# Optimization experiments

Hardware: AMD Instinct MI355X
Metric: run time of the kernel (lower is better)

## Reference

```python
import jax, jax.numpy as jnp
import numpy as np

ALPHA = 0.3  # LeakyReLU negative slope
NEG_INF = -1e9


def setup_inputs() -> dict:
    key = jax.random.key(0)
    k1, k2, k3, k4 = jax.random.split(key, 4)
    B, N, C_IN, C_OUT, H = 4, 2048, 128, 128, 4
    node_feats = jax.random.normal(k1, (B, N, C_IN), dtype=jnp.float32)
    # xavier_uniform with gain 1.414 for projection weight [c_out, c_in]
    limit_w = 1.414 * np.sqrt(6.0 / (C_IN + C_OUT))
    W = jax.random.uniform(k2, (C_OUT, C_IN), minval=-limit_w, maxval=limit_w, dtype=jnp.float32)
    b = jnp.zeros((C_OUT,), dtype=jnp.float32)
    c_head = C_OUT // H
    limit_a = 1.414 * np.sqrt(6.0 / (H + 2 * c_head))
    a = jax.random.uniform(k3, (H, 2 * c_head), minval=-limit_a, maxval=limit_a, dtype=jnp.float32)
    return {"node_feats": node_feats, "W": W, "b": b, "a": a}


def reference(node_feats, W, b, a):
    B, N, _ = node_feats.shape
    H, two_c = a.shape
    c = two_c // 2
    # dynamic adjacency: cosine similarity, sigmoid > 0.5  <=>  sim > 0
    nf = node_feats / jnp.maximum(jnp.linalg.norm(node_feats, axis=-1, keepdims=True), 1e-12)
    sim = jnp.einsum('bid,bjd->bij', nf, nf)            # [B,N,N]
    mask = sim > 0.0                                     # adjacency (sigmoid(sim) > 0.5)
    # projection -> per-head features [B,N,H,c]
    h = (node_feats @ W.T + b).reshape(B, N, H, c)
    # edge score a . [h_i, h_j] decomposes into left/right parts
    a_l, a_r = a[:, :c], a[:, c:]                        # [H,c] each
    s_l = jnp.einsum('bnhc,hc->bnh', h, a_l)             # [B,N,H]
    s_r = jnp.einsum('bnhc,hc->bnh', h, a_r)             # [B,N,H]
    logits = jax.nn.leaky_relu(s_l[:, :, None, :] + s_r[:, None, :, :], ALPHA)  # [B,N,N,H]
    attn = jnp.where(mask[..., None], logits, NEG_INF)
    probs = jax.nn.softmax(attn, axis=2)                 # softmax over source nodes j
    # dropout is identity in eval mode
    out = jnp.einsum('bijh,bjhc->bihc', probs, h)
    return out.reshape(B, N, -1)                         # concat heads
```

## Files before the change

### kernel.cpp

```cpp
#include <hip/hip_runtime.h>
#include <cstdint>
#include <cstddef>

typedef float v16f __attribute__((ext_vector_type(16)));
typedef short v8s  __attribute__((ext_vector_type(8)));

#define MFMA32(A,B,C) __builtin_amdgcn_mfma_f32_32x32x16_bf16((A),(B),(C),0,0,0)
#define THRU 1e-3f
#define SEG 16

__device__ __forceinline__ unsigned f2bf(float f) {
  unsigned u = __builtin_bit_cast(unsigned, f);
  u += 0x7FFFu + ((u >> 16) & 1u);
  return u >> 16;
}
__device__ __forceinline__ float bf2f(unsigned us) {
  return __builtin_bit_cast(float, us << 16);
}
__device__ __forceinline__ void gload16(const void* g, void* l) {
  __builtin_amdgcn_global_load_lds(
      (const __attribute__((address_space(1))) void*)g,
      (__attribute__((address_space(3))) void*)l, 16, 0, 0);
}

__global__ __launch_bounds__(256) void gat_prep(
    const float* __restrict__ nf, const float* __restrict__ Wm,
    const float* __restrict__ bias, const float* __restrict__ aw,
    unsigned short* __restrict__ nfh, unsigned short* __restrict__ nfm,
    unsigned short* __restrict__ ht,
    float* __restrict__ EFl, float* __restrict__ EFrp)
{
  __shared__ float xl[32][132];
  const int tid = threadIdx.x;
  const int row = tid & 31, g = tid >> 5;
  const int r0 = blockIdx.x * 32;
  const int b = r0 >> 11, n0 = r0 & 2047;
  const int d0 = g * 16;

  float x[16];
  {
    const float* xp = nf + (size_t)(r0 + row) * 128 + d0;
#pragma unroll
    for (int q = 0; q < 4; ++q) {
      float4 v = *(const float4*)(xp + 4 * q);
      x[4*q+0] = v.x; x[4*q+1] = v.y; x[4*q+2] = v.z; x[4*q+3] = v.w;
    }
  }
  {
    unsigned hu[16], mu[16];
#pragma unroll
    for (int q = 0; q < 16; ++q) {
      xl[row][d0 + q] = x[q];
      unsigned hb = f2bf(x[q]); float hf = bf2f(hb);
      unsigned mb = f2bf(x[q] - hf);
      hu[q] = hb; mu[q] = mb;
    }
    const size_t to = ((size_t)(b * 64 + (n0 >> 5)) * 8 + g) * 512 + row * 8;
    uint4 p0, p1;
    p0.x = hu[0] | (hu[1] << 16);  p0.y = hu[2] | (hu[3] << 16);
    p0.z = hu[4] | (hu[5] << 16);  p0.w = hu[6] | (hu[7] << 16);
    p1.x = hu[8] | (hu[9] << 16);  p1.y = hu[10] | (hu[11] << 16);
    p1.z = hu[12] | (hu[13] << 16); p1.w = hu[14] | (hu[15] << 16);
    *(uint4*)(nfh + to) = p0; *(uint4*)(nfh + to + 256) = p1;
    p0.x = mu[0] | (mu[1] << 16);  p0.y = mu[2] | (mu[3] << 16);
    p0.z = mu[4] | (mu[5] << 16);  p0.w = mu[6] | (mu[7] << 16);
    p1.x = mu[8] | (mu[9] << 16);  p1.y = mu[10] | (mu[11] << 16);
    p1.z = mu[12] | (mu[13] << 16); p1.w = mu[14] | (mu[15] << 16);
    *(uint4*)(nfm + to) = p0; *(uint4*)(nfm + to + 256) = p1;
  }
  __syncthreads();

  float acc[16];
  const int ob = g * 16;
#pragma unroll
  for (int o = 0; o < 16; ++o) acc[o] = bias[ob + o];
  for (int dd = 0; dd < 128; dd += 4) {
    float4 xq = *(const float4*)&xl[row][dd];
#pragma unroll
    for (int o = 0; o < 16; ++o) {
      float4 wq = *(const float4*)(Wm + (size_t)(ob + o) * 128 + dd);
      acc[o] = fmaf(xq.x, wq.x, acc[o]);
      acc[o] = fmaf(xq.y, wq.y, acc[o]);
      acc[o] = fmaf(xq.z, wq.z, acc[o]);
      acc[o] = fmaf(xq.w, wq.w, acc[o]);
    }
  }
#pragma unroll
  for (int o = 0; o < 16; ++o)
    ht[((size_t)b * 128 + ob + o) * 2048 + n0 + row] = (unsigned short)f2bf(acc[o]);

  const int hh = g >> 1, cb = (g & 1) * 16;
  float sl = 0.f, sr = 0.f;
#pragma unroll
  for (int o = 0; o < 16; ++o) {
    sl = fmaf(acc[o], aw[hh * 64 + cb + o], sl);
    sr = fmaf(acc[o], aw[hh * 64 + 32 + cb + o], sr);
  }
  sl += __shfl_xor(sl, 32, 64);
  sr += __shfl_xor(sr, 32, 64);
  if (!(g & 1)) {
    const float L2E = 1.4426950408889634f;
    float El = exp2f(sl * L2E), Fl = exp2f(sl * (0.3f * L2E));
    float Er = exp2f(sr * L2E), Fr = exp2f(sr * (0.3f * L2E));
    size_t nn = (size_t)(r0 + row);
    EFl[nn * 8 + hh]     = El;
    EFl[nn * 8 + 4 + hh] = Fl;
    EFrp[nn * 8 + (hh >> 1) * 4 + (hh & 1) * 2]     = Er;
    EFrp[nn * 8 + (hh >> 1) * 4 + (hh & 1) * 2 + 1] = Fr;
  }
}

__global__ __launch_bounds__(256) void gat_mask(
    const unsigned short* __restrict__ nfh, const unsigned short* __restrict__ nfm,
    unsigned* __restrict__ mask, unsigned* __restrict__ list,
    unsigned* __restrict__ lcnt)
{
  const int tid = threadIdx.x, lane = tid & 63, wv = tid >> 6;
  const int li = lane & 31, hi = lane >> 5;
  const int blk = blockIdx.x;
  const int jb = blk & 31, t = blk >> 5;
  const int ib = t & 15, b = t >> 4;
  const int i0 = ib * 128 + wv * 32;
  const int j0 = jb * 64;
  const int wid = blk * 4 + wv;

  const size_t lbyte = (size_t)lane * 8;
  const size_t tiB  = ((size_t)(b * 64 + (i0 >> 5)) * 8) * 512 + lbyte;
  const size_t tjA0 = ((size_t)(b * 64 + (j0 >> 5)) * 8) * 512 + lbyte;
  const size_t tjA1 = tjA0 + 4096;

  v8s BH[8], BM[8];
#pragma unroll
  for (int kc = 0; kc < 8; ++kc) {
    BH[kc] = *(const v8s*)(nfh + tiB + kc * 512);
    BM[kc] = *(const v8s*)(nfm + tiB + kc * 512);
  }

  v16f S0, S1;
#pragma unroll
  for (int r = 0; r < 16; ++r) { S0[r] = 0.f; S1[r] = 0.f; }
#pragma unroll
  for (int kc = 0; kc < 8; ++kc) {
    v8s A0h = *(const v8s*)(nfh + tjA0 + kc * 512);
    v8s A1h = *(const v8s*)(nfh + tjA1 + kc * 512);
    v8s A0m = *(const v8s*)(nfm + tjA0 + kc * 512);
    v8s A1m = *(const v8s*)(nfm + tjA1 + kc * 512);
    S0 = MFMA32(A0h, BH[kc], S0);
    S1 = MFMA32(A1h, BH[kc], S1);
    S0 = MFMA32(A0h, BM[kc], S0);
    S1 = MFMA32(A1h, BM[kc], S1);
    S0 = MFMA32(A0m, BH[kc], S0);
    S1 = MFMA32(A1m, BH[kc], S1);
  }

  unsigned u0 = 0, u1 = 0;
  float mn = 1e30f;
  const int sh = hi * 4;
#pragma unroll
  for (int r = 0; r < 16; ++r) {
    const int jlc = (r & 3) + 8 * (r >> 2);
    const unsigned bit = (1u << jlc) << sh;
    if (S0[r] > 0.f) u0 |= bit;
    if (S1[r] > 0.f) u1 |= bit;
    mn = fminf(mn, fabsf(S0[r]));
    mn = fminf(mn, fabsf(S1[r]));
  }
  {
    unsigned f0 = u0 | (unsigned)__shfl_xor((int)u0, 32, 64);
    unsigned f1 = u1 | (unsigned)__shfl_xor((int)u1, 32, 64);
    if (hi == 0) {
      mask[(size_t)(b * 64 + jb * 2)     * 2048 + i0 + li] = f0;
      mask[(size_t)(b * 64 + jb * 2 + 1) * 2048 + i0 + li] = f1;
    }
  }

  int wcount = 0;
  if (__ballot(mn < THRU)) {
#pragma unroll
    for (int sub = 0; sub < 2; ++sub) {
#pragma unroll
      for (int r = 0; r < 16; ++r) {
        const int jl = (r & 3) + 8 * (r >> 2) + 4 * hi;
        const float s = sub ? S1[r] : S0[r];
        const bool f = fabsf(s) < THRU;
        unsigned long long bal = __ballot(f);
        if (bal) {
          if (f) {
            int pos = wcount + (int)__popcll(bal & ((1ull << lane) - 1ull));
            if (pos < SEG)
              list[wid * SEG + pos] =
                  (unsigned)((b << 22) | ((i0 + li) << 11) | (j0 + sub * 32 + jl));
          }
          wcount += (int)__popcll(bal);
        }
      }
    }
    if (wcount > SEG) wcount = SEG;
  }
  if (lane == 0) lcnt[wid] = (unsigned)wcount;
}

__global__ __launch_bounds__(256) void gat_fix(
    const float* __restrict__ nf, const unsigned* __restrict__ list,
    const unsigned* __restrict__ lcnt, unsigned* __restrict__ mask)
{
  const unsigned t = blockIdx.x * 256 + threadIdx.x;
  const unsigned seg = t >> 4, slot = t & (SEG - 1);
  if (slot >= lcnt[seg]) return;
  const unsigned e = list[t];
  const int b = e >> 22, i = (e >> 11) & 2047, j = e & 2047;
  const float* xi = nf + ((size_t)b * 2048 + i) * 128;
  const float* xj = nf + ((size_t)b * 2048 + j) * 128;
  double acc = 0.0;
#pragma unroll 8
  for (int k = 0; k < 128; k += 4) {
    float4 a = *(const float4*)(xi + k);
    float4 c = *(const float4*)(xj + k);
    acc = fma((double)a.x, (double)c.x, acc);
    acc = fma((double)a.y, (double)c.y, acc);
    acc = fma((double)a.z, (double)c.z, acc);
    acc = fma((double)a.w, (double)c.w, acc);
  }
  unsigned* w = &mask[(size_t)(b * 64 + (j >> 5)) * 2048 + i];
  const unsigned bit = 1u << (j & 31);
  if (acc > 0.0) atomicOr(w, bit); else atomicAnd(w, ~bit);
}

#define PVBLK(pw, h, smv)                                                      \
  {                                                                            \
    auto q0 = __builtin_amdgcn_permlane32_swap((int)pw[0], (int)pw[2], false, false); \
    auto q1 = __builtin_amdgcn_permlane32_swap((int)pw[1], (int)pw[3], false, false); \
    auto q2 = __builtin_amdgcn_permlane32_swap((int)pw[4], (int)pw[6], false, false); \
    auto q3 = __builtin_amdgcn_permlane32_swap((int)pw[5], (int)pw[7], false, false); \
    uint4 c0, c1;                                                              \
    c0.x = (unsigned)q0[0]; c0.y = (unsigned)q1[0];                            \
    c0.z = (unsigned)q0[1]; c0.w = (unsigned)q1[1];                            \
    c1.x = (unsigned)q2[0]; c1.y = (unsigned)q3[0];                            \
    c1.z = (unsigned)q2[1]; c1.w = (unsigned)q3[1];                            \
    v8s P0 = __builtin_bit_cast(v8s, c0);                                      \
    v8s P1 = __builtin_bit_cast(v8s, c1);                                      \
    const int cc = (h) * 32 + li;                                              \
    const char* vr = (smv) + cc * 256;                                         \
    const int cx = cc & 15;                                                    \
    v8s V0 = *(const v8s*)(vr + ((((it2 << 2) + hi) ^ cx) << 4));              \
    v8s V1 = *(const v8s*)(vr + ((((it2 << 2) + 2 + hi) ^ cx) << 4));          \
    acc[h] = MFMA32(P0, V0, acc[h]);                                           \
    acc[h] = MFMA32(P1, V1, acc[h]);                                           \
  }

template<int CH>
__global__ __launch_bounds__(256, 2) void gat_attn(
    const unsigned short* __restrict__ ht, const float* __restrict__ EFl,
    const float* __restrict__ EFrp, const unsigned* __restrict__ mask,
    float* __restrict__ nump, float* __restrict__ denp)
{
  constexpr int JPC = 2048 / CH;
  constexpr int H = JPC >> 7;
  constexpr int MW = JPC >> 5;
  __shared__ __align__(16) char sm[2][18432];

  const int tid = threadIdx.x, lane = tid & 63, wv = tid >> 6;
  const int li = lane & 31, hi = lane >> 5;

  const int blk = blockIdx.x;
  const int x = blk & 7, y = blk >> 3;
  const int ig = y & 15;
  const int combo = x * CH + (y >> 4);
  const int hp2 = combo & 1;
  const int r2 = combo >> 1;
  const int ch = r2 % CH, b = r2 / CH;

  const size_t nb = (size_t)b * 2048;
  const int i0 = ig * 128 + wv * 32;
  const int j0 = ch * JPC;

  float EL[2], FL[2];
  {
    const float* p = EFl + (nb + i0 + li) * 8 + 2 * hp2;
    float2 e = *(const float2*)p;
    float2 f = *(const float2*)(p + 4);
    EL[0] = e.x; EL[1] = e.y; FL[0] = f.x; FL[1] = f.y;
  }

  unsigned mw[MW];
#pragma unroll
  for (int q = 0; q < MW; ++q)
    mw[q] = mask[(size_t)(b * 64 + (j0 >> 5) + q) * 2048 + i0 + li] >> (hi * 4);

  v16f acc[2];
#pragma unroll
  for (int h = 0; h < 2; ++h)
#pragma unroll
    for (int r = 0; r < 16; ++r) acc[h][r] = 0.f;
  float den[2] = {0.f, 0.f};

  auto STAGE = [&](int h0, int p) {
    const int jbase = j0 + (h0 << 7);
    const size_t cbase = (size_t)b * 128 + (hp2 << 6);
#pragma unroll
    for (int s = 0; s < 4; ++s) {
      const int L = s * 4096 + tid * 16;
      const int c = L >> 8, gs = (L >> 4) & 15;
      const int g = gs ^ (c & 15);
      gload16((const char*)ht + (((cbase + c) * 2048 + jbase) << 1) + (g << 4),
              sm[p] + L);
    }
    if (tid < 128)
      gload16((const char*)EFrp + (size_t)(nb + jbase + tid) * 32 + (hp2 << 4),
              sm[p] + 16384 + tid * 16);
  };

  STAGE(0, 0);
  __syncthreads();

#pragma unroll
  for (int h0 = 0; h0 < H; ++h0) {
    const int p = h0 & 1;
    if (h0) __syncthreads();
    if (h0 + 1 < H) STAGE(h0 + 1, p ^ 1);

#pragma unroll
    for (int it2 = 0; it2 < 4; ++it2) {
      const char* Eb = sm[p] + 16384 + (it2 << 9);
      const unsigned mh = mw[(h0 << 2) + it2];
      unsigned pA[8], pB[8];
#pragma unroll
      for (int rp = 0; rp < 8; ++rp) {
        const int r0 = 2 * rp;
        const int jl0c = (r0 & 3) + 8 * (r0 >> 2);
        const int nA = (jl0c + 4 * hi) * 16;
        float4 e0 = *(const float4*)(Eb + nA);
        float4 e1 = *(const float4*)(Eb + nA + 16);
        const bool m0 = (mh >> jl0c) & 1;
        const bool m1 = (mh >> (jl0c + 1)) & 1;
        float wA0 = fmaxf(e0.x * EL[0], e0.y * FL[0]); wA0 = m0 ? wA0 : 0.f;
        float wB0 = fmaxf(e0.z * EL[1], e0.w * FL[1]); wB0 = m0 ? wB0 : 0.f;
        float wA1 = fmaxf(e1.x * EL[0], e1.y * FL[0]); wA1 = m1 ? wA1 : 0.f;
        float wB1 = fmaxf(e1.z * EL[1], e1.w * FL[1]); wB1 = m1 ? wB1 : 0.f;
        den[0] += wA0 + wA1;
        den[1] += wB0 + wB1;
        asm("v_cvt_pk_bf16_f32 %0, %1, %2" : "=v"(pA[rp]) : "v"(wA0), "v"(wA1));
        asm("v_cvt_pk_bf16_f32 %0, %1, %2" : "=v"(pB[rp]) : "v"(wB0), "v"(wB1));
      }
      PVBLK(pA, 0, sm[p])
      PVBLK(pB, 1, sm[p])
    }
  }

#pragma unroll
  for (int h = 0; h < 2; ++h) den[h] += __shfl_xor(den[h], 32, 64);

  const size_t obase = ((size_t)b * CH + ch) * 2048 + i0;
#pragma unroll
  for (int h = 0; h < 2; ++h) {
#pragma unroll
    for (int r = 0; r < 16; ++r) {
      const int il = (r & 3) + 8 * (r >> 2) + 4 * hi;
      nump[(obase + il) * 128 + (hp2 * 2 + h) * 32 + li] = acc[h][r];
    }
  }
  if (lane < 32) {
    float2 dv; dv.x = den[0]; dv.y = den[1];
    *(float2*)(denp + (obase + li) * 4 + 2 * hp2) = dv;
  }
}

__global__ __launch_bounds__(256) void gat_reduce(
    const float* __restrict__ nump, const float* __restrict__ denp,
    float* __restrict__ out, const int CH)
{
  const int idx = blockIdx.x * 256 + threadIdx.x;
  const int b = idx >> 18;
  const int rem = idx & 262143;
  const int n = rem >> 7;
  const int col = rem & 127;
  const int h = col >> 5;
  float s = 0.f, d = 0.f;
  for (int ch = 0; ch < CH; ++ch) {
    s += nump[(((size_t)b * CH + ch) * 2048 + n) * 128 + col];
    d += denp[(((size_t)b * CH + ch) * 2048 + n) * 4 + h];
  }
  out[idx] = s / d;
}

extern "C" void kernel_launch(void* const* d_in, const int* in_sizes, int n_in,
                              void* d_out, int out_size, void* d_ws, size_t ws_size,
                              hipStream_t stream) {
  const float* nf   = (const float*)d_in[0];
  const float* Wm   = (const float*)d_in[1];
  const float* bias = (const float*)d_in[2];
  const float* aw   = (const float*)d_in[3];
  float* out = (float*)d_out;
  char* ws = (char*)d_ws;

  unsigned short* nfh  = (unsigned short*)(ws);
  unsigned short* nfm  = (unsigned short*)(ws + 2097152);
  unsigned short* ht   = (unsigned short*)(ws + 4194304);
  float*    EFl  = (float*)(ws + 6291456);
  float*    EFrp = (float*)(ws + 6553600);
  unsigned* mask = (unsigned*)(ws + 6815744);
  unsigned* list = (unsigned*)(ws + 8912896);
  unsigned* lcnt = (unsigned*)(ws + 9437184);
  const size_t o_den = 9469952;

  int CH = 8;
  if (ws_size < o_den + 8ull * 4325376ull) CH = 4;

  float* denp = (float*)(ws + o_den);
  float* nump = (float*)(ws + o_den + (size_t)CH * 131072);

  gat_prep<<<256, 256, 0, stream>>>(nf, Wm, bias, aw, nfh, nfm, ht, EFl, EFrp);
  gat_mask<<<2048, 256, 0, stream>>>(nfh, nfm, mask, list, lcnt);
  gat_fix<<<512, 256, 0, stream>>>(nf, list, lcnt, mask);
  if (CH == 8)
    gat_attn<8><<<1024, 256, 0, stream>>>(ht, EFl, EFrp, mask, nump, denp);
  else
    gat_attn<4><<<512, 256, 0, stream>>>(ht, EFl, EFrp, mask, nump, denp);
  gat_reduce<<<4096, 256, 0, stream>>>(nump, denp, out, CH);
}
```

Baseline: 74.88 us.

## Fuse mask fixup into mask kernel and reduce j-splits inside attention block

The borderline-sign fixup (fp64 dot products for near-zero similarities) moves inline into the mask kernel, which drops the list/count buffers and the separate fix launch. The attention kernel is restructured so each block handles one batch-head pair over 32 rows. Its four waves each take a quarter of the source nodes with per-wave double-buffered async loads synchronised by waitcnt instead of block barriers, then reduce partials through LDS and write normalized output directly. This removes the partial-sum workspace traffic and the reduce kernel, at the cost of divergent fp64 loops in the mask kernel and an LDS reduction at the end of attention.

```diff
diff --git a/kernel.cpp b/kernel.cpp
--- a/kernel.cpp
+++ b/kernel.cpp
@@ -7,7 +7,6 @@
 
 #define MFMA32(A,B,C) __builtin_amdgcn_mfma_f32_32x32x16_bf16((A),(B),(C),0,0,0)
 #define THRU 1e-3f
-#define SEG 16
 
 __device__ __forceinline__ unsigned f2bf(float f) {
   unsigned u = __builtin_bit_cast(unsigned, f);
@@ -28,7 +27,7 @@
     const float* __restrict__ bias, const float* __restrict__ aw,
     unsigned short* __restrict__ nfh, unsigned short* __restrict__ nfm,
     unsigned short* __restrict__ ht,
-    float* __restrict__ EFl, float* __restrict__ EFrp)
+    float* __restrict__ EFl, float* __restrict__ EFh)
 {
   __shared__ float xl[32][132];
   const int tid = threadIdx.x;
@@ -105,24 +104,23 @@
     size_t nn = (size_t)(r0 + row);
     EFl[nn * 8 + hh]     = El;
     EFl[nn * 8 + 4 + hh] = Fl;
-    EFrp[nn * 8 + (hh >> 1) * 4 + (hh & 1) * 2]     = Er;
-    EFrp[nn * 8 + (hh >> 1) * 4 + (hh & 1) * 2 + 1] = Fr;
+    const size_t eo = ((size_t)(b * 4 + hh) * 2048 + (n0 + row)) * 2;
+    EFh[eo]     = Er;
+    EFh[eo + 1] = Fr;
   }
 }
 
 __global__ __launch_bounds__(256) void gat_mask(
     const unsigned short* __restrict__ nfh, const unsigned short* __restrict__ nfm,
-    unsigned* __restrict__ mask, unsigned* __restrict__ list,
-    unsigned* __restrict__ lcnt)
+    const float* __restrict__ nf, unsigned* __restrict__ mask)
 {
-  const int tid = threadIdx.x, lane = tid & 63, wv = tid >> 6;
+  const int tid = threadIdx.x, lane = tid & 63;
   const int li = lane & 31, hi = lane >> 5;
   const int blk = blockIdx.x;
   const int jb = blk & 31, t = blk >> 5;
   const int ib = t & 15, b = t >> 4;
-  const int i0 = ib * 128 + wv * 32;
+  const int i0 = ib * 128 + (tid >> 6) * 32;
   const int j0 = jb * 64;
-  const int wid = blk * 4 + wv;
 
   const size_t lbyte = (size_t)lane * 8;
   const size_t tiB  = ((size_t)(b * 64 + (i0 >> 5)) * 8) * 512 + lbyte;
@@ -165,222 +163,170 @@
     mn = fminf(mn, fabsf(S0[r]));
     mn = fminf(mn, fabsf(S1[r]));
   }
-  {
-    unsigned f0 = u0 | (unsigned)__shfl_xor((int)u0, 32, 64);
-    unsigned f1 = u1 | (unsigned)__shfl_xor((int)u1, 32, 64);
-    if (hi == 0) {
-      mask[(size_t)(b * 64 + jb * 2)     * 2048 + i0 + li] = f0;
-      mask[(size_t)(b * 64 + jb * 2 + 1) * 2048 + i0 + li] = f1;
-    }
-  }
-
-  int wcount = 0;
-  if (__ballot(mn < THRU)) {
+
+  if (mn < THRU) {
+    const float* xi = nf + ((size_t)b * 2048 + i0 + li) * 128;
 #pragma unroll
     for (int sub = 0; sub < 2; ++sub) {
 #pragma unroll
       for (int r = 0; r < 16; ++r) {
-        const int jl = (r & 3) + 8 * (r >> 2) + 4 * hi;
         const float s = sub ? S1[r] : S0[r];
-        const bool f = fabsf(s) < THRU;
-        unsigned long long bal = __ballot(f);
-        if (bal) {
-          if (f) {
-            int pos = wcount + (int)__popcll(bal & ((1ull << lane) - 1ull));
-            if (pos < SEG)
-              list[wid * SEG + pos] =
-                  (unsigned)((b << 22) | ((i0 + li) << 11) | (j0 + sub * 32 + jl));
+        if (fabsf(s) < THRU) {
+          const int jlc = (r & 3) + 8 * (r >> 2);
+          const int j = j0 + sub * 32 + jlc + 4 * hi;
+          const float* xj = nf + ((size_t)b * 2048 + j) * 128;
+          double a = 0.0;
+          for (int k = 0; k < 128; k += 2) {
+            a = fma((double)xi[k],     (double)xj[k],     a);
+            a = fma((double)xi[k + 1], (double)xj[k + 1], a);
           }
-          wcount += (int)__popcll(bal);
+          const unsigned bit = (1u << jlc) << sh;
+          if (sub == 0) u0 = (a > 0.0) ? (u0 | bit) : (u0 & ~bit);
+          else          u1 = (a > 0.0) ? (u1 | bit) : (u1 & ~bit);
         }
       }
     }
-    if (wcount > SEG) wcount = SEG;
-  }
-  if (lane == 0) lcnt[wid] = (unsigned)wcount;
-}
-
-__global__ __launch_bounds__(256) void gat_fix(
-    const float* __restrict__ nf, const unsigned* __restrict__ list,
-    const unsigned* __restrict__ lcnt, unsigned* __restrict__ mask)
-{
-  const unsigned t = blockIdx.x * 256 + threadIdx.x;
-  const unsigned seg = t >> 4, slot = t & (SEG - 1);
-  if (slot >= lcnt[seg]) return;
-  const unsigned e = list[t];
-  const int b = e >> 22, i = (e >> 11) & 2047, j = e & 2047;
-  const float* xi = nf + ((size_t)b * 2048 + i) * 128;
-  const float* xj = nf + ((size_t)b * 2048 + j) * 128;
-  double acc = 0.0;
-#pragma unroll 8
-  for (int k = 0; k < 128; k += 4) {
-    float4 a = *(const float4*)(xi + k);
-    float4 c = *(const float4*)(xj + k);
-    acc = fma((double)a.x, (double)c.x, acc);
-    acc = fma((double)a.y, (double)c.y, acc);
-    acc = fma((double)a.z, (double)c.z, acc);
-    acc = fma((double)a.w, (double)c.w, acc);
-  }
-  unsigned* w = &mask[(size_t)(b * 64 + (j >> 5)) * 2048 + i];
-  const unsigned bit = 1u << (j & 31);
-  if (acc > 0.0) atomicOr(w, bit); else atomicAnd(w, ~bit);
-}
-
-#define PVBLK(pw, h, smv)                                                      \
-  {                                                                            \
-    auto q0 = __builtin_amdgcn_permlane32_swap((int)pw[0], (int)pw[2], false, false); \
-    auto q1 = __builtin_amdgcn_permlane32_swap((int)pw[1], (int)pw[3], false, false); \
-    auto q2 = __builtin_amdgcn_permlane32_swap((int)pw[4], (int)pw[6], false, false); \
-    auto q3 = __builtin_amdgcn_permlane32_swap((int)pw[5], (int)pw[7], false, false); \
-    uint4 c0, c1;                                                              \
-    c0.x = (unsigned)q0[0]; c0.y = (unsigned)q1[0];                            \
-    c0.z = (unsigned)q0[1]; c0.w = (unsigned)q1[1];                            \
-    c1.x = (unsigned)q2[0]; c1.y = (unsigned)q3[0];                            \
-    c1.z = (unsigned)q2[1]; c1.w = (unsigned)q3[1];                            \
-    v8s P0 = __builtin_bit_cast(v8s, c0);                                      \
-    v8s P1 = __builtin_bit_cast(v8s, c1);                                      \
-    const int cc = (h) * 32 + li;                                              \
-    const char* vr = (smv) + cc * 256;                                         \
-    const int cx = cc & 15;                                                    \
-    v8s V0 = *(const v8s*)(vr + ((((it2 << 2) + hi) ^ cx) << 4));              \
-    v8s V1 = *(const v8s*)(vr + ((((it2 << 2) + 2 + hi) ^ cx) << 4));          \
-    acc[h] = MFMA32(P0, V0, acc[h]);                                           \
-    acc[h] = MFMA32(P1, V1, acc[h]);                                           \
-  }
-
-template<int CH>
+  }
+
+  unsigned f0 = u0 | (unsigned)__shfl_xor((int)u0, 32, 64);
+  unsigned f1 = u1 | (unsigned)__shfl_xor((int)u1, 32, 64);
+  if (hi == 0) {
+    mask[(size_t)(b * 64 + jb * 2)     * 2048 + i0 + li] = f0;
+    mask[(size_t)(b * 64 + jb * 2 + 1) * 2048 + i0 + li] = f1;
+  }
+}
+
 __global__ __launch_bounds__(256, 2) void gat_attn(
     const unsigned short* __restrict__ ht, const float* __restrict__ EFl,
-    const float* __restrict__ EFrp, const unsigned* __restrict__ mask,
-    float* __restrict__ nump, float* __restrict__ denp)
+    const float* __restrict__ EFh, const unsigned* __restrict__ mask,
+    float* __restrict__ out)
 {
-  constexpr int JPC = 2048 / CH;
-  constexpr int H = JPC >> 7;
-  constexpr int MW = JPC >> 5;
-  __shared__ __align__(16) char sm[2][18432];
-
+  __shared__ __align__(16) char sm[36864];
   const int tid = threadIdx.x, lane = tid & 63, wv = tid >> 6;
   const int li = lane & 31, hi = lane >> 5;
 
   const int blk = blockIdx.x;
-  const int x = blk & 7, y = blk >> 3;
-  const int ig = y & 15;
-  const int combo = x * CH + (y >> 4);
-  const int hp2 = combo & 1;
-  const int r2 = combo >> 1;
-  const int ch = r2 % CH, b = r2 / CH;
+  const int ig = (blk >> 3) & 63;
+  const int combo = (blk & 7) * 2 + (blk >> 9);
+  const int b = combo >> 2, h = combo & 3;
 
   const size_t nb = (size_t)b * 2048;
-  const int i0 = ig * 128 + wv * 32;
-  const int j0 = ch * JPC;
-
-  float EL[2], FL[2];
-  {
-    const float* p = EFl + (nb + i0 + li) * 8 + 2 * hp2;
-    float2 e = *(const float2*)p;
-    float2 f = *(const float2*)(p + 4);
-    EL[0] = e.x; EL[1] = e.y; FL[0] = f.x; FL[1] = f.y;
-  }
-
-  unsigned mw[MW];
-#pragma unroll
-  for (int q = 0; q < MW; ++q)
-    mw[q] = mask[(size_t)(b * 64 + (j0 >> 5) + q) * 2048 + i0 + li] >> (hi * 4);
-
-  v16f acc[2];
-#pragma unroll
-  for (int h = 0; h < 2; ++h)
-#pragma unroll
-    for (int r = 0; r < 16; ++r) acc[h][r] = 0.f;
-  float den[2] = {0.f, 0.f};
-
+  const int i0 = ig * 32;
+  const int j0w = wv * 512;
+  char* mybase = sm + wv * 9216;
+
+  const float EL = EFl[(nb + i0 + li) * 8 + h];
+  const float FL = EFl[(nb + i0 + li) * 8 + 4 + h];
+
+  unsigned mw[16];
+#pragma unroll
+  for (int q = 0; q < 16; ++q)
+    mw[q] = mask[(size_t)(b * 64 + wv * 16 + q) * 2048 + i0 + li] >> (hi * 4);
+
+  asm volatile("s_waitcnt vmcnt(0)" ::: "memory");
+  __builtin_amdgcn_sched_barrier(0);
+
+  const int vrow = lane >> 3, vgs = lane & 7;
   auto STAGE = [&](int h0, int p) {
-    const int jbase = j0 + (h0 << 7);
-    const size_t cbase = (size_t)b * 128 + (hp2 << 6);
-#pragma unroll
-    for (int s = 0; s < 4; ++s) {
-      const int L = s * 4096 + tid * 16;
-      const int c = L >> 8, gs = (L >> 4) & 15;
-      const int g = gs ^ (c & 15);
-      gload16((const char*)ht + (((cbase + c) * 2048 + jbase) << 1) + (g << 4),
-              sm[p] + L);
-    }
-    if (tid < 128)
-      gload16((const char*)EFrp + (size_t)(nb + jbase + tid) * 32 + (hp2 << 4),
-              sm[p] + 16384 + tid * 16);
+    const int jbase = j0w + (h0 << 6);
+    const size_t srow = (size_t)(b * 128 + h * 32) * 2048 + jbase;
+#pragma unroll
+    for (int q = 0; q < 4; ++q) {
+      const int row = q * 8 + vrow;
+      gload16((const char*)(ht + srow + (size_t)row * 2048 + ((vgs ^ (row & 7)) << 3)),
+              mybase + p * 4608 + q * 1024);
+    }
+    if (lane < 32)
+      gload16((const char*)EFh + ((size_t)(b * 4 + h) * 2048 + jbase) * 8 + lane * 16,
+              mybase + p * 4608 + 4096);
   };
 
   STAGE(0, 0);
-  __syncthreads();
-
-#pragma unroll
-  for (int h0 = 0; h0 < H; ++h0) {
+
+  v16f acc;
+#pragma unroll
+  for (int r = 0; r < 16; ++r) acc[r] = 0.f;
+  float den = 0.f;
+
+#pragma unroll
+  for (int h0 = 0; h0 < 8; ++h0) {
     const int p = h0 & 1;
-    if (h0) __syncthreads();
-    if (h0 + 1 < H) STAGE(h0 + 1, p ^ 1);
-
-#pragma unroll
-    for (int it2 = 0; it2 < 4; ++it2) {
-      const char* Eb = sm[p] + 16384 + (it2 << 9);
-      const unsigned mh = mw[(h0 << 2) + it2];
-      unsigned pA[8], pB[8];
+    if (h0 < 7) {
+      STAGE(h0 + 1, p ^ 1);
+      asm volatile("s_waitcnt vmcnt(5)" ::: "memory");
+    } else {
+      asm volatile("s_waitcnt vmcnt(0)" ::: "memory");
+    }
+    __builtin_amdgcn_sched_barrier(0);
+
+    const char* base = mybase + p * 4608;
+#pragma unroll
+    for (int it2 = 0; it2 < 2; ++it2) {
+      const unsigned mh = mw[h0 * 2 + it2];
+      const char* Eb = base + 4096 + (it2 << 8);
+      unsigned pw[8];
 #pragma unroll
       for (int rp = 0; rp < 8; ++rp) {
         const int r0 = 2 * rp;
         const int jl0c = (r0 & 3) + 8 * (r0 >> 2);
-        const int nA = (jl0c + 4 * hi) * 16;
-        float4 e0 = *(const float4*)(Eb + nA);
-        float4 e1 = *(const float4*)(Eb + nA + 16);
+        const int off = (jl0c + 4 * hi) * 8;
+        float2 e0 = *(const float2*)(Eb + off);
+        float2 e1 = *(const float2*)(Eb + off + 8);
         const bool m0 = (mh >> jl0c) & 1;
         const bool m1 = (mh >> (jl0c + 1)) & 1;
-        float wA0 = fmaxf(e0.x * EL[0], e0.y * FL[0]); wA0 = m0 ? wA0 : 0.f;
-        float wB0 = fmaxf(e0.z * EL[1], e0.w * FL[1]); wB0 = m0 ? wB0 : 0.f;
-        float wA1 = fmaxf(e1.x * EL[0], e1.y * FL[0]); wA1 = m1 ? wA1 : 0.f;
-        float wB1 = fmaxf(e1.z * EL[1], e1.w * FL[1]); wB1 = m1 ? wB1 : 0.f;
-        den[0] += wA0 + wA1;
-        den[1] += wB0 + wB1;
-        asm("v_cvt_pk_bf16_f32 %0, %1, %2" : "=v"(pA[rp]) : "v"(wA0), "v"(wA1));
-        asm("v_cvt_pk_bf16_f32 %0, %1, %2" : "=v"(pB[rp]) : "v"(wB0), "v"(wB1));
+        float w0 = fmaxf(e0.x * EL, e0.y * FL); w0 = m0 ? w0 : 0.f;
+        float w1 = fmaxf(e1.x * EL, e1.y * FL); w1 = m1 ? w1 : 0.f;
+        den += w0 + w1;
+        asm("v_cvt_pk_bf16_f32 %0, %1, %2" : "=v"(pw[rp]) : "v"(w0), "v"(w1));
       }
-      PVBLK(pA, 0, sm[p])
-      PVBLK(pB, 1, sm[p])
-    }
-  }
-
-#pragma unroll
-  for (int h = 0; h < 2; ++h) den[h] += __shfl_xor(den[h], 32, 64);
-
-  const size_t obase = ((size_t)b * CH + ch) * 2048 + i0;
-#pragma unroll
-  for (int h = 0; h < 2; ++h) {
+      auto q0 = __builtin_amdgcn_permlane32_swap((int)pw[0], (int)pw[2], false, false);
+      auto q1 = __builtin_amdgcn_permlane32_swap((int)pw[1], (int)pw[3], false, false);
+      auto q2 = __builtin_amdgcn_permlane32_swap((int)pw[4], (int)pw[6], false, false);
+      auto q3 = __builtin_amdgcn_permlane32_swap((int)pw[5], (int)pw[7], false, false);
+      uint4 c0, c1;
+      c0.x = (unsigned)q0[0]; c0.y = (unsigned)q1[0];
+      c0.z = (unsigned)q0[1]; c0.w = (unsigned)q1[1];
+      c1.x = (unsigned)q2[0]; c1.y = (unsigned)q3[0];
+      c1.z = (unsigned)q2[1]; c1.w = (unsigned)q3[1];
+      v8s P0 = __builtin_bit_cast(v8s, c0);
+      v8s P1 = __builtin_bit_cast(v8s, c1);
+      const char* vr = base + li * 128;
+      const int cx = li & 7;
+      v8s V0 = *(const v8s*)(vr + ((((it2 << 2) + hi) ^ cx) << 4));
+      v8s V1 = *(const v8s*)(vr + ((((it2 << 2) + 2 + hi) ^ cx) << 4));
+      acc = MFMA32(P0, V0, acc);
+      acc = MFMA32(P1, V1, acc);
+    }
+  }
+
+  __syncthreads();
+  if (wv) {
+    float* dst = (float*)sm + (size_t)(wv - 1) * 1088 + lane * 17;
+#pragma unroll
+    for (int r = 0; r < 16; ++r) dst[r] = acc[r];
+    dst[16] = den;
+  }
+  __syncthreads();
+  if (wv == 0) {
+#pragma unroll
+    for (int w = 0; w < 3; ++w) {
+      const float* src = (const float*)sm + (size_t)w * 1088 + lane * 17;
+#pragma unroll
+      for (int r = 0; r < 16; ++r) acc[r] += src[r];
+      den += src[16];
+    }
+    den += __shfl_xor(den, 32, 64);
+    float* dl = (float*)sm + 3 * 1088;
+    if (lane < 32) dl[li] = den;
+    asm volatile("s_waitcnt lgkmcnt(0)" ::: "memory");
+    __builtin_amdgcn_sched_barrier(0);
+    const size_t ob = (nb + i0) * 128 + h * 32 + li;
 #pragma unroll
     for (int r = 0; r < 16; ++r) {
       const int il = (r & 3) + 8 * (r >> 2) + 4 * hi;
-      nump[(obase + il) * 128 + (hp2 * 2 + h) * 32 + li] = acc[h][r];
-    }
-  }
-  if (lane < 32) {
-    float2 dv; dv.x = den[0]; dv.y = den[1];
-    *(float2*)(denp + (obase + li) * 4 + 2 * hp2) = dv;
-  }
-}
-
-__global__ __launch_bounds__(256) void gat_reduce(
-    const float* __restrict__ nump, const float* __restrict__ denp,
-    float* __restrict__ out, const int CH)
-{
-  const int idx = blockIdx.x * 256 + threadIdx.x;
-  const int b = idx >> 18;
-  const int rem = idx & 262143;
-  const int n = rem >> 7;
-  const int col = rem & 127;
-  const int h = col >> 5;
-  float s = 0.f, d = 0.f;
-  for (int ch = 0; ch < CH; ++ch) {
-    s += nump[(((size_t)b * CH + ch) * 2048 + n) * 128 + col];
-    d += denp[(((size_t)b * CH + ch) * 2048 + n) * 4 + h];
-  }
-  out[idx] = s / d;
+      out[ob + (size_t)il * 128] = acc[r] / dl[il];
+    }
+  }
 }
 
 extern "C" void kernel_launch(void* const* d_in, const int* in_sizes, int n_in,
@@ -393,28 +339,14 @@
   float* out = (float*)d_out;
   char* ws = (char*)d_ws;
 
-  unsigned short* nfh  = (unsigned short*)(ws);
-  unsigned short* nfm  = (unsigned short*)(ws + 2097152);
-  unsigned short* ht   = (unsigned short*)(ws + 4194304);
+  unsigned short* nfh = (unsigned short*)(ws);
+  unsigned short* nfm = (unsigned short*)(ws + 2097152);
+  unsigned short* ht  = (unsigned short*)(ws + 4194304);
   float*    EFl  = (float*)(ws + 6291456);
-  float*    EFrp = (float*)(ws + 6553600);
+  float*    EFh  = (float*)(ws + 6553600);
   unsigned* mask = (unsigned*)(ws + 6815744);
-  unsigned* list = (unsigned*)(ws + 8912896);
-  unsigned* lcnt = (unsigned*)(ws + 9437184);
-  const size_t o_den = 9469952;
-
-  int CH = 8;
-  if (ws_size < o_den + 8ull * 4325376ull) CH = 4;
-
-  float* denp = (float*)(ws + o_den);
-  float* nump = (float*)(ws + o_den + (size_t)CH * 131072);
-
-  gat_prep<<<256, 256, 0, stream>>>(nf, Wm, bias, aw, nfh, nfm, ht, EFl, EFrp);
-  gat_mask<<<2048, 256, 0, stream>>>(nfh, nfm, mask, list, lcnt);
-  gat_fix<<<512, 256, 0, stream>>>(nf, list, lcnt, mask);
-  if (CH == 8)
-    gat_attn<8><<<1024, 256, 0, stream>>>(ht, EFl, EFrp, mask, nump, denp);
-  else
-    gat_attn<4><<<512, 256, 0, stream>>>(ht, EFl, EFrp, mask, nump, denp);
-  gat_reduce<<<4096, 256, 0, stream>>>(nump, denp, out, CH);
-}
+
+  gat_prep<<<256, 256, 0, stream>>>(nf, Wm, bias, aw, nfh, nfm, ht, EFl, EFh);
+  gat_mask<<<2048, 256, 0, stream>>>(nfh, nfm, nf, mask);
+  gat_attn<<<1024, 256, 0, stream>>>(ht, EFl, EFh, mask, out);
+}
```

Result: slower. 82.10 us (+9.6%).

## Fuse near-zero similarity fixup into mask kernel and vectorize reduce

Applied to the files above, without the earlier changes.

Drops the separate list/fixup kernel. The mask kernel now recomputes ambiguous near-zero similarity entries in place, in double precision, before writing the mask bits. This removes one launch, the list/count buffers and the atomics. The trade-off is divergent per-lane scalar double loops inside the MFMA kernel, with no cap on how many entries get fixed. The reduce kernel is also switched to float4 loads and stores, with a quarter of the threads.

```diff
diff --git a/kernel.cpp b/kernel.cpp
--- a/kernel.cpp
+++ b/kernel.cpp
@@ -7,7 +7,6 @@
 
 #define MFMA32(A,B,C) __builtin_amdgcn_mfma_f32_32x32x16_bf16((A),(B),(C),0,0,0)
 #define THRU 1e-3f
-#define SEG 16
 
 __device__ __forceinline__ unsigned f2bf(float f) {
   unsigned u = __builtin_bit_cast(unsigned, f);
@@ -112,17 +111,15 @@
 
 __global__ __launch_bounds__(256) void gat_mask(
     const unsigned short* __restrict__ nfh, const unsigned short* __restrict__ nfm,
-    unsigned* __restrict__ mask, unsigned* __restrict__ list,
-    unsigned* __restrict__ lcnt)
+    const float* __restrict__ nf, unsigned* __restrict__ mask)
 {
-  const int tid = threadIdx.x, lane = tid & 63, wv = tid >> 6;
+  const int tid = threadIdx.x, lane = tid & 63;
   const int li = lane & 31, hi = lane >> 5;
   const int blk = blockIdx.x;
   const int jb = blk & 31, t = blk >> 5;
   const int ib = t & 15, b = t >> 4;
-  const int i0 = ib * 128 + wv * 32;
+  const int i0 = ib * 128 + (tid >> 6) * 32;
   const int j0 = jb * 64;
-  const int wid = blk * 4 + wv;
 
   const size_t lbyte = (size_t)lane * 8;
   const size_t tiB  = ((size_t)(b * 64 + (i0 >> 5)) * 8) * 512 + lbyte;
@@ -165,65 +162,37 @@
     mn = fminf(mn, fabsf(S0[r]));
     mn = fminf(mn, fabsf(S1[r]));
   }
-  {
-    unsigned f0 = u0 | (unsigned)__shfl_xor((int)u0, 32, 64);
-    unsigned f1 = u1 | (unsigned)__shfl_xor((int)u1, 32, 64);
-    if (hi == 0) {
-      mask[(size_t)(b * 64 + jb * 2)     * 2048 + i0 + li] = f0;
-      mask[(size_t)(b * 64 + jb * 2 + 1) * 2048 + i0 + li] = f1;
-    }
-  }
-
-  int wcount = 0;
-  if (__ballot(mn < THRU)) {
+
+  if (mn < THRU) {
+    const float* xi = nf + ((size_t)b * 2048 + i0 + li) * 128;
 #pragma unroll
     for (int sub = 0; sub < 2; ++sub) {
 #pragma unroll
       for (int r = 0; r < 16; ++r) {
-        const int jl = (r & 3) + 8 * (r >> 2) + 4 * hi;
         const float s = sub ? S1[r] : S0[r];
-        const bool f = fabsf(s) < THRU;
-        unsigned long long bal = __ballot(f);
-        if (bal) {
-          if (f) {
-            int pos = wcount + (int)__popcll(bal & ((1ull << lane) - 1ull));
-            if (pos < SEG)
-              list[wid * SEG + pos] =
-                  (unsigned)((b << 22) | ((i0 + li) << 11) | (j0 + sub * 32 + jl));
+        if (fabsf(s) < THRU) {
+          const int jlc = (r & 3) + 8 * (r >> 2);
+          const int j = j0 + sub * 32 + jlc + 4 * hi;
+          const float* xj = nf + ((size_t)b * 2048 + j) * 128;
+          double a = 0.0;
+          for (int k = 0; k < 128; k += 2) {
+            a = fma((double)xi[k],     (double)xj[k],     a);
+            a = fma((double)xi[k + 1], (double)xj[k + 1], a);
           }
-          wcount += (int)__popcll(bal);
+          const unsigned bit = (1u << jlc) << sh;
+          if (sub == 0) u0 = (a > 0.0) ? (u0 | bit) : (u0 & ~bit);
+          else          u1 = (a > 0.0) ? (u1 | bit) : (u1 & ~bit);
         }
       }
     }
-    if (wcount > SEG) wcount = SEG;
-  }
-  if (lane == 0) lcnt[wid] = (unsigned)wcount;
-}
-
-__global__ __launch_bounds__(256) void gat_fix(
-    const float* __restrict__ nf, const unsigned* __restrict__ list,
-    const unsigned* __restrict__ lcnt, unsigned* __restrict__ mask)
-{
-  const unsigned t = blockIdx.x * 256 + threadIdx.x;
-  const unsigned seg = t >> 4, slot = t & (SEG - 1);
-  if (slot >= lcnt[seg]) return;
-  const unsigned e = list[t];
-  const int b = e >> 22, i = (e >> 11) & 2047, j = e & 2047;
-  const float* xi = nf + ((size_t)b * 2048 + i) * 128;
-  const float* xj = nf + ((size_t)b * 2048 + j) * 128;
-  double acc = 0.0;
-#pragma unroll 8
-  for (int k = 0; k < 128; k += 4) {
-    float4 a = *(const float4*)(xi + k);
-    float4 c = *(const float4*)(xj + k);
-    acc = fma((double)a.x, (double)c.x, acc);
-    acc = fma((double)a.y, (double)c.y, acc);
-    acc = fma((double)a.z, (double)c.z, acc);
-    acc = fma((double)a.w, (double)c.w, acc);
-  }
-  unsigned* w = &mask[(size_t)(b * 64 + (j >> 5)) * 2048 + i];
-  const unsigned bit = 1u << (j & 31);
-  if (acc > 0.0) atomicOr(w, bit); else atomicAnd(w, ~bit);
+  }
+
+  unsigned f0 = u0 | (unsigned)__shfl_xor((int)u0, 32, 64);
+  unsigned f1 = u1 | (unsigned)__shfl_xor((int)u1, 32, 64);
+  if (hi == 0) {
+    mask[(size_t)(b * 64 + jb * 2)     * 2048 + i0 + li] = f0;
+    mask[(size_t)(b * 64 + jb * 2 + 1) * 2048 + i0 + li] = f1;
+  }
 }
 
 #define PVBLK(pw, h, smv)                                                      \
@@ -369,18 +338,23 @@
     const float* __restrict__ nump, const float* __restrict__ denp,
     float* __restrict__ out, const int CH)
 {
-  const int idx = blockIdx.x * 256 + threadIdx.x;
-  const int b = idx >> 18;
-  const int rem = idx & 262143;
-  const int n = rem >> 7;
-  const int col = rem & 127;
+  const int t = blockIdx.x * 256 + threadIdx.x;
+  const int b = t >> 16;
+  const int rem = t & 65535;
+  const int n = rem >> 5;
+  const int col = (rem & 31) * 4;
   const int h = col >> 5;
-  float s = 0.f, d = 0.f;
+  float4 s = make_float4(0.f, 0.f, 0.f, 0.f);
+  float d = 0.f;
   for (int ch = 0; ch < CH; ++ch) {
-    s += nump[(((size_t)b * CH + ch) * 2048 + n) * 128 + col];
-    d += denp[(((size_t)b * CH + ch) * 2048 + n) * 4 + h];
-  }
-  out[idx] = s / d;
+    const size_t rb = ((size_t)b * CH + ch) * 2048 + n;
+    float4 v = *(const float4*)(nump + rb * 128 + col);
+    s.x += v.x; s.y += v.y; s.z += v.z; s.w += v.w;
+    d += denp[rb * 4 + h];
+  }
+  float4 o;
+  o.x = s.x / d; o.y = s.y / d; o.z = s.z / d; o.w = s.w / d;
+  *(float4*)(out + (size_t)t * 4) = o;
 }
 
 extern "C" void kernel_launch(void* const* d_in, const int* in_sizes, int n_in,
@@ -399,9 +373,7 @@
   float*    EFl  = (float*)(ws + 6291456);
   float*    EFrp = (float*)(ws + 6553600);
   unsigned* mask = (unsigned*)(ws + 6815744);
-  unsigned* list = (unsigned*)(ws + 8912896);
-  unsigned* lcnt = (unsigned*)(ws + 9437184);
-  const size_t o_den = 9469952;
+  const size_t o_den = 8912896;
 
   int CH = 8;
   if (ws_size < o_den + 8ull * 4325376ull) CH = 4;
@@ -410,11 +382,10 @@
   float* nump = (float*)(ws + o_den + (size_t)CH * 131072);
 
   gat_prep<<<256, 256, 0, stream>>>(nf, Wm, bias, aw, nfh, nfm, ht, EFl, EFrp);
-  gat_mask<<<2048, 256, 0, stream>>>(nfh, nfm, mask, list, lcnt);
-  gat_fix<<<512, 256, 0, stream>>>(nf, list, lcnt, mask);
+  gat_mask<<<2048, 256, 0, stream>>>(nfh, nfm, nf, mask);
   if (CH == 8)
     gat_attn<8><<<1024, 256, 0, stream>>>(ht, EFl, EFrp, mask, nump, denp);
   else
     gat_attn<4><<<512, 256, 0, stream>>>(ht, EFl, EFrp, mask, nump, denp);
-  gat_reduce<<<4096, 256, 0, stream>>>(nump, denp, out, CH);
-}
+  gat_reduce<<<1024, 256, 0, stream>>>(nump, denp, out, CH);
+}
```

New measurement: 76.24 us. About the same (+1.8%).
